# Performance work log

Hardware: AMD Instinct MI355X
Metric: run time of the kernel (lower is better)

The kernel has to match this reference:

```python
import jax, jax.numpy as jnp
import numpy as np

DN = ('NCHW', 'OIHW', 'NCHW')
EPS = 1e-5


def _conv(x, w, b, stride, pad):
    y = jax.lax.conv_general_dilated(x, w, (stride, stride), ((pad, pad), (pad, pad)), dimension_numbers=DN)
    return y + b[None, :, None, None]


def _convT(x, w, b):
    # PyTorch ConvTranspose2d(k=4, s=2, p=1); w: (Cin, Cout, 4, 4)
    k = jnp.flip(w, (2, 3)).transpose(1, 0, 2, 3)  # -> (Cout, Cin, 4, 4)
    y = jax.lax.conv_general_dilated(x, k, (1, 1), ((2, 2), (2, 2)), lhs_dilation=(2, 2), dimension_numbers=DN)
    return y + b[None, :, None, None]


def _bn(x, g, b):
    # training-mode BatchNorm2d: batch stats over (N, H, W)
    m = x.mean((0, 2, 3), keepdims=True)
    v = x.var((0, 2, 3), keepdims=True)
    return (x - m) * jax.lax.rsqrt(v + EPS) * g[None, :, None, None] + b[None, :, None, None]


def _resblock(x, g1, b1, w3, b3, g2, b2, w1, b1c):
    h = jax.nn.relu(_bn(x, g1, b1))
    h = _conv(h, w3, b3, 1, 1)
    h = jax.nn.relu(_bn(h, g2, b2))
    h = _conv(h, w1, b1c, 1, 0)
    return h + x


def setup_inputs() -> dict:
    B, C, H, W, D, K = 16, 3, 128, 128, 256, 512
    key = jax.random.key(0)
    ks = iter(jax.random.split(key, 16))
    s = 0.05
    inp = {
        'x': jax.random.normal(next(ks), (B, C, H, W), jnp.float32),
        'ec1_w': jax.random.normal(next(ks), (D, C, 4, 4), jnp.float32) * s,
        'ec1_b': jnp.zeros((D,), jnp.float32),
        'ebn1_g': jnp.ones((D,), jnp.float32),
        'ebn1_b': jnp.zeros((D,), jnp.float32),
        'ec2_w': jax.random.normal(next(ks), (D, D, 4, 4), jnp.float32) * s,
        'ec2_b': jnp.zeros((D,), jnp.float32),
        # 4 residual blocks stacked: [0,1]=encoder, [2,3]=decoder
        'rb_bn1_g': jnp.ones((4, D), jnp.float32),
        'rb_bn1_b': jnp.zeros((4, D), jnp.float32),
        'rb_c3_w': jax.random.normal(next(ks), (4, D, D, 3, 3), jnp.float32) * s,
        'rb_c3_b': jnp.zeros((4, D), jnp.float32),
        'rb_bn2_g': jnp.ones((4, D), jnp.float32),
        'rb_bn2_b': jnp.zeros((4, D), jnp.float32),
        'rb_c1_w': jax.random.normal(next(ks), (4, D, D, 1, 1), jnp.float32) * s,
        'rb_c1_b': jnp.zeros((4, D), jnp.float32),
        'dbn1_g': jnp.ones((D,), jnp.float32),
        'dbn1_b': jnp.zeros((D,), jnp.float32),
        'dct1_w': jax.random.normal(next(ks), (D, D, 4, 4), jnp.float32) * s,  # (Cin, Cout, kH, kW)
        'dct1_b': jnp.zeros((D,), jnp.float32),
        'dbn2_g': jnp.ones((D,), jnp.float32),
        'dbn2_b': jnp.zeros((D,), jnp.float32),
        'dct2_w': jax.random.normal(next(ks), (D, C, 4, 4), jnp.float32) * s,
        'dct2_b': jnp.zeros((C,), jnp.float32),
        'codebook': jax.random.uniform(next(ks), (K, D), jnp.float32, -1.0 / K, 1.0 / K),
    }
    return inp


def reference(x, ec1_w, ec1_b, ebn1_g, ebn1_b, ec2_w, ec2_b,
              rb_bn1_g, rb_bn1_b, rb_c3_w, rb_c3_b, rb_bn2_g, rb_bn2_b, rb_c1_w, rb_c1_b,
              dbn1_g, dbn1_b, dct1_w, dct1_b, dbn2_g, dbn2_b, dct2_w, dct2_b, codebook):
    def rb(h, i):
        return _resblock(h, rb_bn1_g[i], rb_bn1_b[i], rb_c3_w[i], rb_c3_b[i],
                         rb_bn2_g[i], rb_bn2_b[i], rb_c1_w[i], rb_c1_b[i])

    # Encoder
    h = _conv(x, ec1_w, ec1_b, 2, 1)
    h = jax.nn.relu(_bn(h, ebn1_g, ebn1_b))
    h = _conv(h, ec2_w, ec2_b, 2, 1)
    h = rb(h, 0)
    z_e = rb(h, 1)  # [N, D, H/4, W/4]

    # Vector quantizer: argmin_k sum_d (z - w_k)^2 via norm expansion
    N, D, Hh, Ww = z_e.shape
    ze_f = z_e.transpose(0, 2, 3, 1).reshape(-1, D)  # [M, D]
    d2 = ((ze_f ** 2).sum(1, keepdims=True)
          - 2.0 * ze_f @ codebook.T
          + (codebook ** 2).sum(1)[None, :])  # [M, K]
    q = jnp.argmin(d2, axis=1)
    z_q = codebook[q].reshape(N, Hh, Ww, D).transpose(0, 3, 1, 2)

    # Decoder (takes z_e, per original forward)
    d = rb(z_e, 2)
    d = rb(d, 3)
    d = jax.nn.relu(_bn(d, dbn1_g, dbn1_b))
    d = _convT(d, dct1_w, dct1_b)
    d = jax.nn.relu(_bn(d, dbn2_g, dbn2_b))
    x_rec = _convT(d, dct2_w, dct2_b)

    return (x_rec, z_e, z_q)
```

## Files before the change

### kernel.cpp

```cpp
#include <hip/hip_runtime.h>
#include <stdint.h>

typedef __bf16 bf16_t;
typedef __bf16 bf16x8 __attribute__((ext_vector_type(8)));
typedef float f32x4 __attribute__((ext_vector_type(4)));

#define DEVINL __device__ __forceinline__

DEVINL float bf2f(bf16_t h){ return (float)h; }
DEVINL bf16_t f2bf(float f){ return (bf16_t)f; }

DEVINL void g2l16(const void* g, void* l){
  __builtin_amdgcn_global_load_lds(
      (const __attribute__((address_space(1))) uint32_t*)g,
      (__attribute__((address_space(3))) uint32_t*)l, 16, 0, 0);
}

#define SB_BYTES    9469952
#define SB0_OFF     35684352
#define STATS_OFF   73564160
#define CBN_OFF     73586688
#define WP_OFF      73588736
#define XI_OFF      83353600
#define WS_NEEDED   91742208
#define WP_RB3(i) (1048576 + (i)*655360)
#define WP_RB1(i) (1048576 + (i)*655360 + 589824)
#define WP_CT     3670016
#define WP_CB     4718592
#define WP_EC1    4849664
#define WP_CT2    4866048
#define WP_ELEMS  4882432

DEVINL void zerohalo_one(bf16_t* buf, int IW, int idx){
  int g8 = idx & 31, r = idx >> 5;
  int H = 4*IW - 4;
  int nn = r / H, hp = r - nn*H;
  int y, x;
  if (hp < IW){ y = 0; x = hp; }
  else if (hp < 2*IW){ y = IW-1; x = hp - IW; }
  else {
    int h2 = hp - 2*IW;
    int side = h2 / (IW-2);
    int k = h2 - side*(IW-2);
    y = k + 1; x = side ? (IW-1) : 0;
  }
  bf16_t* p = buf + ((size_t)((nn*IW + y)*IW + x))*256 + g8*8;
  bf16x8 zv;
#pragma unroll
  for (int e = 0; e < 8; e++) zv[e] = f2bf(0.f);
  *(bf16x8*)p = zv;
}

__global__ __launch_bounds__(256) void k_prep(bf16_t* __restrict__ A64, bf16_t* __restrict__ SB,
                                              uint4* __restrict__ statz){
  int b = blockIdx.x, t = threadIdx.x;
  if (b < 521){
    int idx = b*256 + t;
    if (idx < 133120) zerohalo_one(A64, 66, idx);
  } else if (b < 1577){
    int r = b - 521;
    int buf = r / 264, li = r - buf*264;
    int idx = li*256 + t;
    if (idx < 67584) zerohalo_one(SB + (size_t)buf*(SB_BYTES/2), 34, idx);
  } else {
    int i = (b - 1577)*256 + t;
    if (i < 1408) statz[i] = make_uint4(0,0,0,0);
  }
}

__global__ __launch_bounds__(256) void k_repack(
    const float* __restrict__ ec2_w, const float* __restrict__ rb_c3_w,
    const float* __restrict__ rb_c1_w, const float* __restrict__ dct1_w,
    const float* __restrict__ codebook, const float* __restrict__ ec1_w,
    const float* __restrict__ dct2_w, bf16_t* __restrict__ wp, float* __restrict__ cbn)
{
  int idx = blockIdx.x*256 + threadIdx.x;
  if (idx >= WP_ELEMS){
    int k = idx - WP_ELEMS;
    if (k < 512){
      float s = 0.f;
      for (int d = 0; d < 256; d++){ float v = codebook[k*256 + d]; s += v*v; }
      cbn[k] = s;
    }
    return;
  }
  int l = idx; float v;
  if (l < 1048576) {
    int t = l>>16, co = (l>>8)&255, ci = l&255;
    v = ec2_w[co*4096 + ci*16 + t];
  } else {
    l -= 1048576;
    if (l < 2621440) {
      int i = l / 655360;
      int r = l - i*655360;
      if (r < 589824) {
        int t = r>>16, co = (r>>8)&255, ci = r&255;
        v = rb_c3_w[i*589824 + co*2304 + ci*9 + t];
      } else {
        r -= 589824;
        int co = r>>8, ci = r&255;
        v = rb_c1_w[i*65536 + co*256 + ci];
      }
    } else {
      l -= 2621440;
      if (l < 1048576) {
        int z = l>>18, r = l&262143, t = r>>16, co = (r>>8)&255, ci = r&255;
        int py = z>>1, px = z&1, a = t>>1, b = t&1;
        int ky = 2*a + 1 - py, kx = 2*b + 1 - px;
        v = dct1_w[ci*4096 + co*16 + ky*4 + kx];
      } else {
        l -= 1048576;
        if (l < 131072) {
          v = codebook[l];
        } else {
          l -= 131072;
          if (l < 16384){
            int co = l>>6, k = l&63;
            v = (k < 48) ? ec1_w[co*48 + k] : 0.f;
          } else {
            l -= 16384;
            int n = l>>8, ci = l&255;
            v = (n < 48) ? dct2_w[ci*48 + n] : 0.f;
          }
        }
      }
    }
  }
  wp[idx] = f2bf(v);
}

__global__ __launch_bounds__(256) void k_im2col(const float* __restrict__ x, bf16_t* __restrict__ Xi){
  int m = blockIdx.x*256 + threadIdx.x;
  int nn = m >> 12, oy = (m >> 6) & 63, ox = m & 63;
  bf16_t row[64];
#pragma unroll
  for (int k = 48; k < 64; k++) row[k] = f2bf(0.f);
#pragma unroll
  for (int ci = 0; ci < 3; ci++)
#pragma unroll
    for (int ky = 0; ky < 4; ky++){
      int iy = 2*oy + ky - 1;
      bool yok = (unsigned)iy < 128u;
#pragma unroll
      for (int kx = 0; kx < 4; kx++){
        int ix = 2*ox + kx - 1;
        float v = (yok && (unsigned)ix < 128u) ? x[((size_t)((nn*3+ci)*128 + iy))*128 + ix] : 0.f;
        row[ci*16 + ky*4 + kx] = f2bf(v);
      }
    }
#pragma unroll
  for (int u = 0; u < 8; u++){
    bf16x8 o;
#pragma unroll
    for (int e = 0; e < 8; e++) o[e] = row[u*8+e];
    *(bf16x8*)(Xi + (size_t)m*64 + u*8) = o;
  }
}

__global__ __launch_bounds__(256) void k_bnapply(const bf16_t* __restrict__ in, bf16_t* __restrict__ out,
    const float* __restrict__ stat, const float* __restrict__ g, const float* __restrict__ b,
    int hwlog, float invc)
{
  int idx = blockIdx.x*256 + threadIdx.x;
  int g8 = idx & 31, p = idx >> 5;
  int HW = 1 << hwlog, IW = HW + 2;
  int xx = p & (HW-1), yy = (p >> hwlog) & (HW-1), nn = p >> (2*hwlog);
  size_t a = ((size_t)((nn*IW + yy+1)*IW + xx+1))*256 + g8*8;
  float sm[8], sq[8], gv[8], bv[8];
#pragma unroll
  for (int e = 0; e < 8; e += 4){
    *(float4*)(sm+e) = *(const float4*)(stat + g8*8 + e);
    *(float4*)(sq+e) = *(const float4*)(stat + 256 + g8*8 + e);
    *(float4*)(gv+e) = *(const float4*)(g + g8*8 + e);
    *(float4*)(bv+e) = *(const float4*)(b + g8*8 + e);
  }
  bf16x8 v = *(const bf16x8*)(in + a);
  bf16x8 o;
#pragma unroll
  for (int e = 0; e < 8; e++){
    float mean = sm[e]*invc;
    float var  = sq[e]*invc - mean*mean;
    float sc = gv[e] * rsqrtf(var + 1e-5f);
    float sh = bv[e] - mean*sc;
    o[e] = f2bf(fmaxf(bf2f(v[e])*sc + sh, 0.f));
  }
  *(bf16x8*)(out + a) = o;
}

template<int MODE>
__global__ __launch_bounds__(256) void k_gemm(
    const bf16_t* __restrict__ in, const bf16_t* __restrict__ wp,
    const float* __restrict__ bias, const bf16_t* __restrict__ res,
    bf16_t* __restrict__ outb, float* __restrict__ outf,
    float* __restrict__ stat, int out_mode, float alpha)
{
  constexpr int TAPS = (MODE==0)?16:(MODE==1)?9:(MODE==3)?4:1;
  constexpr int CHUNKS = (MODE==5)?1:TAPS*4;
  const int N = gridDim.y * 64;

  __shared__ __align__(16) bf16_t As[128*64];
  __shared__ __align__(16) bf16_t Bs[64*64];
  __shared__ float s_sum[64], s_sum2[64];

  const int tid  = threadIdx.x;
  const int lane = tid & 63;
  const int wave = tid >> 6;
  const int m0   = blockIdx.x * 128;
  const int n0   = blockIdx.y * 64;
  int py = 0, px = 0;
  const bf16_t* wpp = wp;
  if (MODE == 3){ py = blockIdx.z >> 1; px = blockIdx.z & 1; wpp += (size_t)blockIdx.z * 262144; }

  int abase[4];
#pragma unroll
  for (int j = 0; j < 4; j++){
    int s = j*256 + wave*64 + lane;
    int row = s >> 3, ug = (s & 7) ^ (row & 7);
    int m = m0 + row;
    int pbase;
    if (MODE == 0){ int nn=m>>10, sp=m&1023, oy=sp>>5, ox=sp&31; pbase = (nn*66 + 2*oy)*66 + 2*ox; }
    else if (MODE == 3){ int nn=m>>10, sp=m&1023, oy=sp>>5, ox=sp&31; pbase = (nn*34 + oy+1+py)*34 + ox+1+px; }
    else if (MODE == 5){ pbase = 0; }
    else if (MODE == 6){ int nn=m>>12, oy=(m>>6)&63, ox=m&63; pbase = (nn*66 + oy+1)*66 + ox+1; }
    else { int nn=m>>10, sp=m&1023, oy=sp>>5, ox=sp&31; pbase = (nn*34 + oy)*34 + ox; }
    abase[j] = (MODE==5) ? (m*64 + ug*8) : (pbase*256 + ug*8);
  }
  int bbase[2];
#pragma unroll
  for (int j = 0; j < 2; j++){
    int s = j*256 + wave*64 + lane;
    int row = s >> 3, ug = (s & 7) ^ (row & 7);
    bbase[j] = (MODE==5) ? ((n0+row)*64 + ug*8) : ((n0+row)*256 + ug*8);
  }

  f32x4 acc[4][2];
#pragma unroll
  for (int i = 0; i < 4; i++)
#pragma unroll
    for (int j = 0; j < 2; j++) acc[i][j] = (f32x4){0.f,0.f,0.f,0.f};

  const int rowbase = (wave >> 1) * 64;
  const int colbase = (wave & 1) * 32;
  const int mf = lane & 15;
  const int kq = lane >> 4;

  for (int c = 0; c < CHUNKS; ++c){
    int t = (MODE==5) ? 0 : (c >> 2);
    int koff;
    if (MODE == 0)      koff = ((t >> 2)*66 + (t & 3))*256 + ((c&3)<<6);
    else if (MODE == 1){ int ky = t/3; koff = (ky*34 + (t - ky*3))*256 + ((c&3)<<6); }
    else if (MODE == 2) koff = 35*256 + ((c&3)<<6);
    else if (MODE == 3) koff = -((t >> 1)*34 + (t & 1))*256 + ((c&3)<<6);
    else if (MODE == 6) koff = ((c&3)<<6);
    else                koff = 0;
    size_t bko = (MODE==5) ? 0 : ((size_t)t*N*256 + ((c&3)<<6));
#pragma unroll
    for (int j = 0; j < 4; j++)
      g2l16(in + abase[j] + koff, As + (j*256 + wave*64)*8);
#pragma unroll
    for (int j = 0; j < 2; j++)
      g2l16(wpp + bko + bbase[j], Bs + (j*256 + wave*64)*8);
    __syncthreads();

#pragma unroll
    for (int kk = 0; kk < 2; kk++){
      bf16x8 af[4], bfr[2];
#pragma unroll
      for (int i = 0; i < 4; i++){
        int rr = rowbase + i*16 + mf;
        af[i] = *reinterpret_cast<const bf16x8*>(&As[rr*64 + (((kk*4+kq) ^ (rr&7))<<3)]);
      }
#pragma unroll
      for (int j = 0; j < 2; j++){
        int rr = colbase + j*16 + mf;
        bfr[j] = *reinterpret_cast<const bf16x8*>(&Bs[rr*64 + (((kk*4+kq) ^ (rr&7))<<3)]);
      }
#pragma unroll
      for (int i = 0; i < 4; i++)
#pragma unroll
        for (int j = 0; j < 2; j++)
          acc[i][j] = __builtin_amdgcn_mfma_f32_16x16x32_bf16(af[i], bfr[j], acc[i][j], 0, 0, 0);
    }
    __syncthreads();
  }

  float psum[2] = {0.f, 0.f}, psum2[2] = {0.f, 0.f};
  const int rowq = (lane >> 4) * 4;
#pragma unroll
  for (int i = 0; i < 4; i++){
#pragma unroll
    for (int r = 0; r < 4; r++){
      int m = m0 + rowbase + i*16 + rowq + r;
      int nn, oy, ox;
      if (MODE == 5){ nn = m >> 12; oy = (m >> 6) & 63; ox = m & 63; }
      else { nn = m >> 10; oy = (m >> 5) & 31; ox = m & 31; }
#pragma unroll
      for (int j = 0; j < 2; j++){
        int co = n0 + colbase + j*16 + mf;
        float v = alpha * acc[i][j][r] + (bias ? bias[co] : 0.f);
        if (res) v += bf2f(res[((size_t)((nn*34 + oy+1)*34 + ox+1))*256 + co]);
        psum[j] += v; psum2[j] += v*v;
        if (out_mode == 2){
          outf[(size_t)m * N + co] = v;
        } else if (MODE == 3){
          outb[((size_t)((nn*66 + 2*oy+py+1)*66 + 2*ox+px+1))*256 + co] = f2bf(v);
        } else if (MODE == 5){
          outb[((size_t)((nn*66 + oy+1)*66 + ox+1))*256 + co] = f2bf(v);
        } else {
          outb[((size_t)((nn*34 + oy+1)*34 + ox+1))*256 + co] = f2bf(v);
          if (out_mode == 1)
            outf[(size_t)nn*262144 + (size_t)co*1024 + oy*32 + ox] = v;
        }
      }
    }
  }
  if (stat){
    if (tid < 64){ s_sum[tid] = 0.f; s_sum2[tid] = 0.f; }
    __syncthreads();
#pragma unroll
    for (int j = 0; j < 2; j++){
      int cl = colbase + j*16 + mf;
      atomicAdd(&s_sum[cl], psum[j]);
      atomicAdd(&s_sum2[cl], psum2[j]);
    }
    __syncthreads();
    if (tid < 64){
      atomicAdd(&stat[n0 + tid], s_sum[tid]);
      atomicAdd(&stat[256 + n0 + tid], s_sum2[tid]);
    }
  }
}

__global__ __launch_bounds__(256) void k_vq_argmin(const float* __restrict__ scores,
    const float* __restrict__ cb, float* __restrict__ zq)
{
  __shared__ int best[32];
  __shared__ float Z[32*256];
  int tid = threadIdx.x, lane = tid & 63, wave = tid >> 6;
  int m0 = blockIdx.x * 32;
  int nn = m0 >> 10, y = (m0 >> 5) & 31;
  for (int rr = wave; rr < 32; rr += 4){
    const float* srow = scores + (size_t)(m0 + rr) * 512;
    float bv = 3.4e38f; int bk = 0;
    for (int k = lane; k < 512; k += 64){
      float v = srow[k];
      if (v < bv){ bv = v; bk = k; }
    }
    for (int off = 32; off; off >>= 1){
      float ov = __shfl_down(bv, off);
      int   ok = __shfl_down(bk, off);
      if (ov < bv || (ov == bv && ok < bk)){ bv = ov; bk = ok; }
    }
    if (lane == 0) best[rr] = bk;
  }
  __syncthreads();
  for (int rr = 0; rr < 32; rr++)
    Z[rr*256 + tid] = cb[best[rr]*256 + tid];
  __syncthreads();
  float* orow = zq + (size_t)nn*262144 + (size_t)tid*1024 + y*32;
#pragma unroll
  for (int x4 = 0; x4 < 8; x4++){
    float4 v;
    v.x = Z[(x4*4+0)*256 + tid];
    v.y = Z[(x4*4+1)*256 + tid];
    v.z = Z[(x4*4+2)*256 + tid];
    v.w = Z[(x4*4+3)*256 + tid];
    *(float4*)(orow + x4*4) = v;
  }
}

__global__ __launch_bounds__(256) void k_ct2asm(const float* __restrict__ P,
    const float* __restrict__ bias, float* __restrict__ out)
{
  int idx = blockIdx.x*256 + threadIdx.x;
  int nn = idx >> 14, oy2 = (idx >> 7) & 127, ox2 = idx & 127;
  int py = oy2 & 1, px = ox2 & 1, oyh = oy2 >> 1, oxh = ox2 >> 1;
  float a0 = bias[0], a1 = bias[1], a2 = bias[2];
#pragma unroll
  for (int a = 0; a < 2; a++){
    int iy = oyh + py - a;
    if ((unsigned)iy > 63u) continue;
    int ky = 2*a + 1 - py;
#pragma unroll
    for (int b = 0; b < 2; b++){
      int ix = oxh + px - b;
      if ((unsigned)ix > 63u) continue;
      int kx = 2*b + 1 - px;
      const float* pr = P + ((size_t)(nn*4096 + iy*64 + ix))*64 + ky*4 + kx;
      a0 += pr[0]; a1 += pr[16]; a2 += pr[32];
    }
  }
  size_t o = (size_t)nn*49152 + (size_t)oy2*128 + ox2;
  out[o]         = a0;
  out[o + 16384] = a1;
  out[o + 32768] = a2;
}

extern "C" void kernel_launch(void* const* d_in, const int* in_sizes, int n_in,
                              void* d_out, int out_size, void* d_ws, size_t ws_size,
                              hipStream_t stream)
{
  if (ws_size < (size_t)WS_NEEDED) return;

  const float* x       = (const float*)d_in[0];
  const float* ec1_w   = (const float*)d_in[1];
  const float* ec1_b   = (const float*)d_in[2];
  const float* ebn1_g  = (const float*)d_in[3];
  const float* ebn1_b  = (const float*)d_in[4];
  const float* ec2_w   = (const float*)d_in[5];
  const float* ec2_b   = (const float*)d_in[6];
  const float* rb_bn1_g= (const float*)d_in[7];
  const float* rb_bn1_b= (const float*)d_in[8];
  const float* rb_c3_w = (const float*)d_in[9];
  const float* rb_c3_b = (const float*)d_in[10];
  const float* rb_bn2_g= (const float*)d_in[11];
  const float* rb_bn2_b= (const float*)d_in[12];
  const float* rb_c1_w = (const float*)d_in[13];
  const float* rb_c1_b = (const float*)d_in[14];
  const float* dbn1_g  = (const float*)d_in[15];
  const float* dbn1_b  = (const float*)d_in[16];
  const float* dct1_w  = (const float*)d_in[17];
  const float* dct1_b  = (const float*)d_in[18];
  const float* dbn2_g  = (const float*)d_in[19];
  const float* dbn2_b  = (const float*)d_in[20];
  const float* dct2_w  = (const float*)d_in[21];
  const float* dct2_b  = (const float*)d_in[22];
  const float* codebook= (const float*)d_in[23];

  char* ws = (char*)d_ws;
  bf16_t* A64 = (bf16_t*)ws;
  float*  scores = (float*)ws;
  bf16_t* SB0 = (bf16_t*)(ws + SB0_OFF);
  bf16_t* SB1 = (bf16_t*)(ws + SB0_OFF + 1*SB_BYTES);
  bf16_t* SB2 = (bf16_t*)(ws + SB0_OFF + 2*SB_BYTES);
  bf16_t* SB3 = (bf16_t*)(ws + SB0_OFF + 3*SB_BYTES);
  float*  P   = (float*)(ws + SB0_OFF + 1*SB_BYTES);
  float*  stats = (float*)(ws + STATS_OFF);
  float*  cbn   = (float*)(ws + CBN_OFF);
  bf16_t* Wp    = (bf16_t*)(ws + WP_OFF);
  bf16_t* Xi    = (bf16_t*)(ws + XI_OFF);

  float* xrec = (float*)d_out;
  float* zef  = xrec + 786432;
  float* zqf  = zef + 4194304;

  k_prep  <<<dim3(1583),  256, 0, stream>>>(A64, SB0, (uint4*)(ws + STATS_OFF));
  k_repack<<<dim3(19074), 256, 0, stream>>>(ec2_w, rb_c3_w, rb_c1_w, dct1_w, codebook,
                                            ec1_w, dct2_w, Wp, cbn);

  k_im2col<<<dim3(256), 256, 0, stream>>>(x, Xi);
  k_gemm<5><<<dim3(512,4,1), 256, 0, stream>>>(Xi, Wp + WP_EC1, ec1_b, nullptr, A64, nullptr,
                                               stats, 0, 1.f);
  k_bnapply<<<dim3(8192), 256, 0, stream>>>(A64, A64, stats, ebn1_g, ebn1_b, 6, 1.f/65536.f);
  k_gemm<0><<<dim3(128,4,1), 256, 0, stream>>>(A64, Wp, ec2_b, nullptr, SB0, nullptr,
                                               stats + 1*512, 0, 1.f);

  auto launch_rb = [&](bf16_t* xin, bf16_t* xout, int i, int sIn, int sMid, int sOut, float* zf){
    k_bnapply<<<dim3(2048), 256, 0, stream>>>(xin, SB1, stats + sIn*512,
                                              rb_bn1_g + i*256, rb_bn1_b + i*256, 5, 1.f/16384.f);
    k_gemm<1><<<dim3(128,4,1), 256, 0, stream>>>(SB1, Wp + WP_RB3(i), rb_c3_b + i*256,
                                                 nullptr, SB2, nullptr, stats + sMid*512, 0, 1.f);
    k_bnapply<<<dim3(2048), 256, 0, stream>>>(SB2, SB2, stats + sMid*512,
                                              rb_bn2_g + i*256, rb_bn2_b + i*256, 5, 1.f/16384.f);
    k_gemm<2><<<dim3(128,4,1), 256, 0, stream>>>(SB2, Wp + WP_RB1(i), rb_c1_b + i*256,
                                                 xin, xout, zf, stats + sOut*512, zf ? 1 : 0, 1.f);
  };

  launch_rb(SB0, SB3, 0, 1, 2, 3, nullptr);
  launch_rb(SB3, SB0, 1, 3, 4, 5, zef);

  k_gemm<2><<<dim3(128,8,1), 256, 0, stream>>>(SB0, Wp + WP_CB, cbn, nullptr, nullptr, scores,
                                               nullptr, 2, -2.f);
  k_vq_argmin<<<dim3(512), 256, 0, stream>>>(scores, codebook, zqf);

  launch_rb(SB0, SB3, 2, 5, 6, 7, nullptr);
  launch_rb(SB3, SB0, 3, 7, 8, 9, nullptr);

  k_bnapply<<<dim3(2048), 256, 0, stream>>>(SB0, SB0, stats + 9*512, dbn1_g, dbn1_b, 5, 1.f/16384.f);
  k_gemm<3><<<dim3(128,4,4), 256, 0, stream>>>(SB0, Wp + WP_CT, dct1_b, nullptr, A64, nullptr,
                                               stats + 10*512, 0, 1.f);

  k_bnapply<<<dim3(8192), 256, 0, stream>>>(A64, A64, stats + 10*512, dbn2_g, dbn2_b, 6, 1.f/65536.f);
  k_gemm<6><<<dim3(512,1,1), 256, 0, stream>>>(A64, Wp + WP_CT2, nullptr, nullptr, nullptr, P,
                                               nullptr, 2, 1.f);
  k_ct2asm<<<dim3(1024), 256, 0, stream>>>(P, dct2_b, xrec);
}
```

Before: 733.8 us.

## Add halo-tiled implicit-GEMM conv kernel reusing LDS input across taps

Adds a k_conv kernel for the strided 4x4 conv, the 3x3 residual convs and the transposed conv. Each block stages a spatial input tile with its halo for one channel chunk in LDS once, then loops over all taps from that tile, instead of reloading the A tile from global memory for every tap. Weights are read straight from global memory into registers with a one-step prefetch rather than through LDS. k_gemm is reduced to the 1x1 and plain GEMM modes. The trade-offs are more LDS per block, a new XOR swizzle scheme and weight traffic that now hits global memory or cache on every tap.

```diff
diff --git a/kernel.cpp b/kernel.cpp
--- a/kernel.cpp
+++ b/kernel.cpp
@@ -188,14 +188,154 @@
 }
 
 template<int MODE>
+__global__ __launch_bounds__(256) void k_conv(
+    const bf16_t* __restrict__ in, const bf16_t* __restrict__ wp,
+    const float* __restrict__ bias, bf16_t* __restrict__ outb,
+    float* __restrict__ stat)
+{
+  constexpr int TAPS = (MODE==0)?16:(MODE==1)?9:4;
+  constexpr int UPP  = (MODE==0)?4:8;
+  constexpr int BK   = UPP*8;
+  constexpr int KK   = BK/32;
+  constexpr int NCH  = 256/BK;
+  constexpr int PXPAD= (MODE==0)?672:(MODE==1)?208:176;
+  constexpr int TU   = PXPAD*UPP;
+  constexpr int UPPL = (MODE==0)?2:3;
+
+  __shared__ __align__(16) bf16_t As[PXPAD*BK];
+  __shared__ float s_sum[64], s_sum2[64];
+
+  const int tid = threadIdx.x, lane = tid & 63, wave = tid >> 6;
+  const int nn = blockIdx.x >> 3, y0 = (blockIdx.x & 7) << 2;
+  const int n0 = blockIdx.y * 64;
+  int ppy = 0, ppx = 0;
+  const bf16_t* wpp = wp;
+  if (MODE == 3){ ppy = blockIdx.z >> 1; ppx = blockIdx.z & 1; wpp += (size_t)blockIdx.z * 262144; }
+
+  size_t wbase;
+  if (MODE == 0)      wbase = (size_t)((nn*66 + 2*y0)*66) * 256;
+  else if (MODE == 1) wbase = (size_t)((nn*34 + y0)*34) * 256;
+  else                wbase = (size_t)((nn*34 + y0 + ppy)*34) * 256;
+
+  const int rowbase = (wave >> 1) * 64;
+  const int colbase = (wave & 1) * 32;
+  const int mf = lane & 15;
+  const int kq = lane >> 4;
+
+  int pxb[4];
+#pragma unroll
+  for (int i = 0; i < 4; i++){
+    int ml = rowbase + i*16 + mf;
+    int yl = ml >> 5, xl = ml & 31;
+    if (MODE == 0)      pxb[i] = (2*yl)*66 + 2*xl;
+    else if (MODE == 1) pxb[i] = yl*34 + xl;
+    else                pxb[i] = (yl+1)*34 + xl + 1 + ppx;
+  }
+
+  f32x4 acc[4][2];
+#pragma unroll
+  for (int i = 0; i < 4; i++)
+#pragma unroll
+    for (int j = 0; j < 2; j++) acc[i][j] = (f32x4){0.f,0.f,0.f,0.f};
+
+  const bf16_t* bcol0 = wpp + (size_t)(n0 + colbase + mf)*256;
+
+  for (int c = 0; c < NCH; c++){
+    const int ch0 = c * BK;
+#pragma unroll
+    for (int g = 0; g < TU/64; g++){
+      int gg = g*64;
+      if ((gg & 255) != wave*64) continue;
+      int s = gg + lane;
+      int px = s >> UPPL, u = s & (UPP-1);
+      int key = (MODE == 0) ? ((px >> 1) & 3) : (px & 7);
+      g2l16(in + wbase + (size_t)px*256 + ch0 + ((u ^ key) << 3), As + (size_t)s*8);
+    }
+    bf16x8 b0c, b1c;
+    {
+      const bf16_t* bp = bcol0 + ch0 + (kq << 3);
+      b0c = *(const bf16x8*)bp;
+      b1c = *(const bf16x8*)(bp + 4096);
+    }
+    __syncthreads();
+#pragma unroll
+    for (int tk = 0; tk < TAPS*KK; tk++){
+      const int t = (KK == 2) ? (tk >> 1) : tk;
+      const int u = (KK == 2) ? ((tk & 1)*4 + kq) : kq;
+      bf16x8 b0n, b1n;
+      if (tk + 1 < TAPS*KK){
+        int t2 = (KK == 2) ? ((tk+1) >> 1) : (tk+1);
+        int u2 = (KK == 2) ? (((tk+1) & 1)*4 + kq) : kq;
+        const bf16_t* bp = bcol0 + (size_t)t2*65536 + ch0 + (u2 << 3);
+        b0n = *(const bf16x8*)bp;
+        b1n = *(const bf16x8*)(bp + 4096);
+      }
+      int to;
+      if (MODE == 0)      to = (t >> 2)*66 + (t & 3);
+      else if (MODE == 1) to = (t/3)*34 + (t - (t/3)*3);
+      else                to = -((t >> 1)*34 + (t & 1));
+      bf16x8 af[4];
+#pragma unroll
+      for (int i = 0; i < 4; i++){
+        int px = pxb[i] + to;
+        int key = (MODE == 0) ? ((px >> 1) & 3) : (px & 7);
+        af[i] = *reinterpret_cast<const bf16x8*>(&As[(size_t)px*BK + ((u ^ key) << 3)]);
+      }
+#pragma unroll
+      for (int i = 0; i < 4; i++){
+        acc[i][0] = __builtin_amdgcn_mfma_f32_16x16x32_bf16(af[i], b0c, acc[i][0], 0, 0, 0);
+        acc[i][1] = __builtin_amdgcn_mfma_f32_16x16x32_bf16(af[i], b1c, acc[i][1], 0, 0, 0);
+      }
+      b0c = b0n; b1c = b1n;
+    }
+    __syncthreads();
+  }
+
+  float psum[2] = {0.f, 0.f}, psum2[2] = {0.f, 0.f};
+  const int rowq = (lane >> 4) * 4;
+#pragma unroll
+  for (int i = 0; i < 4; i++){
+#pragma unroll
+    for (int r = 0; r < 4; r++){
+      int ml = rowbase + i*16 + rowq + r;
+      int y = y0 + (ml >> 5), x = ml & 31;
+#pragma unroll
+      for (int j = 0; j < 2; j++){
+        int co = n0 + colbase + j*16 + mf;
+        float v = acc[i][j][r] + bias[co];
+        psum[j] += v; psum2[j] += v*v;
+        if (MODE == 3)
+          outb[((size_t)((nn*66 + 2*y+ppy+1)*66 + 2*x+ppx+1))*256 + co] = f2bf(v);
+        else
+          outb[((size_t)((nn*34 + y+1)*34 + x+1))*256 + co] = f2bf(v);
+      }
+    }
+  }
+  if (stat){
+    if (tid < 64){ s_sum[tid] = 0.f; s_sum2[tid] = 0.f; }
+    __syncthreads();
+#pragma unroll
+    for (int j = 0; j < 2; j++){
+      int cl = colbase + j*16 + mf;
+      atomicAdd(&s_sum[cl], psum[j]);
+      atomicAdd(&s_sum2[cl], psum2[j]);
+    }
+    __syncthreads();
+    if (tid < 64){
+      atomicAdd(&stat[n0 + tid], s_sum[tid]);
+      atomicAdd(&stat[256 + n0 + tid], s_sum2[tid]);
+    }
+  }
+}
+
+template<int MODE>
 __global__ __launch_bounds__(256) void k_gemm(
     const bf16_t* __restrict__ in, const bf16_t* __restrict__ wp,
     const float* __restrict__ bias, const bf16_t* __restrict__ res,
     bf16_t* __restrict__ outb, float* __restrict__ outf,
     float* __restrict__ stat, int out_mode, float alpha)
 {
-  constexpr int TAPS = (MODE==0)?16:(MODE==1)?9:(MODE==3)?4:1;
-  constexpr int CHUNKS = (MODE==5)?1:TAPS*4;
+  constexpr int CHUNKS = (MODE==5)?1:4;
   const int N = gridDim.y * 64;
 
   __shared__ __align__(16) bf16_t As[128*64];
@@ -207,9 +347,6 @@
   const int wave = tid >> 6;
   const int m0   = blockIdx.x * 128;
   const int n0   = blockIdx.y * 64;
-  int py = 0, px = 0;
-  const bf16_t* wpp = wp;
-  if (MODE == 3){ py = blockIdx.z >> 1; px = blockIdx.z & 1; wpp += (size_t)blockIdx.z * 262144; }
 
   int abase[4];
 #pragma unroll
@@ -218,11 +355,9 @@
     int row = s >> 3, ug = (s & 7) ^ (row & 7);
     int m = m0 + row;
     int pbase;
-    if (MODE == 0){ int nn=m>>10, sp=m&1023, oy=sp>>5, ox=sp&31; pbase = (nn*66 + 2*oy)*66 + 2*ox; }
-    else if (MODE == 3){ int nn=m>>10, sp=m&1023, oy=sp>>5, ox=sp&31; pbase = (nn*34 + oy+1+py)*34 + ox+1+px; }
-    else if (MODE == 5){ pbase = 0; }
+    if (MODE == 5){ pbase = 0; }
     else if (MODE == 6){ int nn=m>>12, oy=(m>>6)&63, ox=m&63; pbase = (nn*66 + oy+1)*66 + ox+1; }
-    else { int nn=m>>10, sp=m&1023, oy=sp>>5, ox=sp&31; pbase = (nn*34 + oy)*34 + ox; }
+    else { int nn=m>>10, sp=m&1023, oy=sp>>5, ox=sp&31; pbase = (nn*34 + oy+1)*34 + ox+1; }
     abase[j] = (MODE==5) ? (m*64 + ug*8) : (pbase*256 + ug*8);
   }
   int bbase[2];
@@ -245,21 +380,13 @@
   const int kq = lane >> 4;
 
   for (int c = 0; c < CHUNKS; ++c){
-    int t = (MODE==5) ? 0 : (c >> 2);
-    int koff;
-    if (MODE == 0)      koff = ((t >> 2)*66 + (t & 3))*256 + ((c&3)<<6);
-    else if (MODE == 1){ int ky = t/3; koff = (ky*34 + (t - ky*3))*256 + ((c&3)<<6); }
-    else if (MODE == 2) koff = 35*256 + ((c&3)<<6);
-    else if (MODE == 3) koff = -((t >> 1)*34 + (t & 1))*256 + ((c&3)<<6);
-    else if (MODE == 6) koff = ((c&3)<<6);
-    else                koff = 0;
-    size_t bko = (MODE==5) ? 0 : ((size_t)t*N*256 + ((c&3)<<6));
+    int koff = (MODE==5) ? 0 : (c<<6);
 #pragma unroll
     for (int j = 0; j < 4; j++)
       g2l16(in + abase[j] + koff, As + (j*256 + wave*64)*8);
 #pragma unroll
     for (int j = 0; j < 2; j++)
-      g2l16(wpp + bko + bbase[j], Bs + (j*256 + wave*64)*8);
+      g2l16(wp + koff + bbase[j], Bs + (j*256 + wave*64)*8);
     __syncthreads();
 
 #pragma unroll
@@ -302,8 +429,6 @@
         psum[j] += v; psum2[j] += v*v;
         if (out_mode == 2){
           outf[(size_t)m * N + co] = v;
-        } else if (MODE == 3){
-          outb[((size_t)((nn*66 + 2*oy+py+1)*66 + 2*ox+px+1))*256 + co] = f2bf(v);
         } else if (MODE == 5){
           outb[((size_t)((nn*66 + oy+1)*66 + ox+1))*256 + co] = f2bf(v);
         } else {
@@ -452,14 +577,13 @@
   k_gemm<5><<<dim3(512,4,1), 256, 0, stream>>>(Xi, Wp + WP_EC1, ec1_b, nullptr, A64, nullptr,
                                                stats, 0, 1.f);
   k_bnapply<<<dim3(8192), 256, 0, stream>>>(A64, A64, stats, ebn1_g, ebn1_b, 6, 1.f/65536.f);
-  k_gemm<0><<<dim3(128,4,1), 256, 0, stream>>>(A64, Wp, ec2_b, nullptr, SB0, nullptr,
-                                               stats + 1*512, 0, 1.f);
+  k_conv<0><<<dim3(128,4), 256, 0, stream>>>(A64, Wp, ec2_b, SB0, stats + 1*512);
 
   auto launch_rb = [&](bf16_t* xin, bf16_t* xout, int i, int sIn, int sMid, int sOut, float* zf){
     k_bnapply<<<dim3(2048), 256, 0, stream>>>(xin, SB1, stats + sIn*512,
                                               rb_bn1_g + i*256, rb_bn1_b + i*256, 5, 1.f/16384.f);
-    k_gemm<1><<<dim3(128,4,1), 256, 0, stream>>>(SB1, Wp + WP_RB3(i), rb_c3_b + i*256,
-                                                 nullptr, SB2, nullptr, stats + sMid*512, 0, 1.f);
+    k_conv<1><<<dim3(128,4), 256, 0, stream>>>(SB1, Wp + WP_RB3(i), rb_c3_b + i*256,
+                                               SB2, stats + sMid*512);
     k_bnapply<<<dim3(2048), 256, 0, stream>>>(SB2, SB2, stats + sMid*512,
                                               rb_bn2_g + i*256, rb_bn2_b + i*256, 5, 1.f/16384.f);
     k_gemm<2><<<dim3(128,4,1), 256, 0, stream>>>(SB2, Wp + WP_RB1(i), rb_c1_b + i*256,
@@ -477,8 +601,7 @@
   launch_rb(SB3, SB0, 3, 7, 8, 9, nullptr);
 
   k_bnapply<<<dim3(2048), 256, 0, stream>>>(SB0, SB0, stats + 9*512, dbn1_g, dbn1_b, 5, 1.f/16384.f);
-  k_gemm<3><<<dim3(128,4,4), 256, 0, stream>>>(SB0, Wp + WP_CT, dct1_b, nullptr, A64, nullptr,
-                                               stats + 10*512, 0, 1.f);
+  k_conv<3><<<dim3(128,4,4), 256, 0, stream>>>(SB0, Wp + WP_CT, dct1_b, A64, stats + 10*512);
 
   k_bnapply<<<dim3(8192), 256, 0, stream>>>(A64, A64, stats + 10*512, dbn2_g, dbn2_b, 6, 1.f/65536.f);
   k_gemm<6><<<dim3(512,1,1), 256, 0, stream>>>(A64, Wp + WP_CT2, nullptr, nullptr, nullptr, P,
```

After: 779.3 us. 6.2% more time.

## Double-buffer GEMM LDS tiles to overlap global loads with MFMA

Applied to the files above, without the earlier changes.

Splits the A and B shared-memory tiles into two buffers. The next chunk's global-to-LDS loads are issued before computing on the current chunk, and completion is tracked with explicit vmcnt waits and raw barriers instead of __syncthreads. Tap offset computation moves into a staging lambda, and the MODE 2 centre offset is folded into abase. The aim is to hide global load latency behind the matrix instructions, at the cost of doubled LDS per block and possibly lower occupancy. It also changes MODE 6 epilogue indexing to a 64x64 spatial layout.

```diff
diff --git a/kernel.cpp b/kernel.cpp
--- a/kernel.cpp
+++ b/kernel.cpp
@@ -198,8 +198,8 @@
   constexpr int CHUNKS = (MODE==5)?1:TAPS*4;
   const int N = gridDim.y * 64;
 
-  __shared__ __align__(16) bf16_t As[128*64];
-  __shared__ __align__(16) bf16_t Bs[64*64];
+  __shared__ __align__(16) bf16_t As[2][128*64];
+  __shared__ __align__(16) bf16_t Bs[2][64*64];
   __shared__ float s_sum[64], s_sum2[64];
 
   const int tid  = threadIdx.x;
@@ -207,9 +207,9 @@
   const int wave = tid >> 6;
   const int m0   = blockIdx.x * 128;
   const int n0   = blockIdx.y * 64;
-  int py = 0, px = 0;
+  int ppy = 0, ppx = 0;
   const bf16_t* wpp = wp;
-  if (MODE == 3){ py = blockIdx.z >> 1; px = blockIdx.z & 1; wpp += (size_t)blockIdx.z * 262144; }
+  if (MODE == 3){ ppy = blockIdx.z >> 1; ppx = blockIdx.z & 1; wpp += (size_t)blockIdx.z * 262144; }
 
   int abase[4];
 #pragma unroll
@@ -219,10 +219,11 @@
     int m = m0 + row;
     int pbase;
     if (MODE == 0){ int nn=m>>10, sp=m&1023, oy=sp>>5, ox=sp&31; pbase = (nn*66 + 2*oy)*66 + 2*ox; }
-    else if (MODE == 3){ int nn=m>>10, sp=m&1023, oy=sp>>5, ox=sp&31; pbase = (nn*34 + oy+1+py)*34 + ox+1+px; }
+    else if (MODE == 1){ int nn=m>>10, sp=m&1023, oy=sp>>5, ox=sp&31; pbase = (nn*34 + oy)*34 + ox; }
+    else if (MODE == 3){ int nn=m>>10, sp=m&1023, oy=sp>>5, ox=sp&31; pbase = (nn*34 + oy+1+ppy)*34 + ox+1+ppx; }
     else if (MODE == 5){ pbase = 0; }
     else if (MODE == 6){ int nn=m>>12, oy=(m>>6)&63, ox=m&63; pbase = (nn*66 + oy+1)*66 + ox+1; }
-    else { int nn=m>>10, sp=m&1023, oy=sp>>5, ox=sp&31; pbase = (nn*34 + oy)*34 + ox; }
+    else { int nn=m>>10, sp=m&1023, oy=sp>>5, ox=sp&31; pbase = (nn*34 + oy+1)*34 + ox+1; }
     abase[j] = (MODE==5) ? (m*64 + ug*8) : (pbase*256 + ug*8);
   }
   int bbase[2];
@@ -233,6 +234,22 @@
     bbase[j] = (MODE==5) ? ((n0+row)*64 + ug*8) : ((n0+row)*256 + ug*8);
   }
 
+  auto stage = [&](int buf, int c){
+    int t = c >> 2;
+    int koff, bko;
+    if (MODE == 0){ koff = ((t>>2)*66 + (t&3))*256 + ((c&3)<<6); bko = t*65536 + ((c&3)<<6); }
+    else if (MODE == 1){ int ky = t/3; koff = (ky*34 + (t - ky*3))*256 + ((c&3)<<6); bko = t*65536 + ((c&3)<<6); }
+    else if (MODE == 3){ koff = -(((t>>1)*34 + (t&1))*256) + ((c&3)<<6); bko = t*65536 + ((c&3)<<6); }
+    else if (MODE == 5){ koff = 0; bko = 0; }
+    else { koff = (c&3)<<6; bko = (c&3)<<6; }
+#pragma unroll
+    for (int j = 0; j < 4; j++)
+      g2l16(in + abase[j] + koff, &As[buf][(j*256 + wave*64)*8]);
+#pragma unroll
+    for (int j = 0; j < 2; j++)
+      g2l16(wpp + bko + bbase[j], &Bs[buf][(j*256 + wave*64)*8]);
+  };
+
   f32x4 acc[4][2];
 #pragma unroll
   for (int i = 0; i < 4; i++)
@@ -244,23 +261,16 @@
   const int mf = lane & 15;
   const int kq = lane >> 4;
 
+  stage(0, 0);
   for (int c = 0; c < CHUNKS; ++c){
-    int t = (MODE==5) ? 0 : (c >> 2);
-    int koff;
-    if (MODE == 0)      koff = ((t >> 2)*66 + (t & 3))*256 + ((c&3)<<6);
-    else if (MODE == 1){ int ky = t/3; koff = (ky*34 + (t - ky*3))*256 + ((c&3)<<6); }
-    else if (MODE == 2) koff = 35*256 + ((c&3)<<6);
-    else if (MODE == 3) koff = -((t >> 1)*34 + (t & 1))*256 + ((c&3)<<6);
-    else if (MODE == 6) koff = ((c&3)<<6);
-    else                koff = 0;
-    size_t bko = (MODE==5) ? 0 : ((size_t)t*N*256 + ((c&3)<<6));
-#pragma unroll
-    for (int j = 0; j < 4; j++)
-      g2l16(in + abase[j] + koff, As + (j*256 + wave*64)*8);
-#pragma unroll
-    for (int j = 0; j < 2; j++)
-      g2l16(wpp + bko + bbase[j], Bs + (j*256 + wave*64)*8);
-    __syncthreads();
+    const int cur = c & 1;
+    if (c + 1 < CHUNKS){
+      stage(cur ^ 1, c + 1);
+      asm volatile("s_waitcnt vmcnt(6)" ::: "memory");
+    } else {
+      asm volatile("s_waitcnt vmcnt(0)" ::: "memory");
+    }
+    asm volatile("s_barrier" ::: "memory");
 
 #pragma unroll
     for (int kk = 0; kk < 2; kk++){
@@ -268,12 +278,12 @@
 #pragma unroll
       for (int i = 0; i < 4; i++){
         int rr = rowbase + i*16 + mf;
-        af[i] = *reinterpret_cast<const bf16x8*>(&As[rr*64 + (((kk*4+kq) ^ (rr&7))<<3)]);
+        af[i] = *reinterpret_cast<const bf16x8*>(&As[cur][rr*64 + (((kk*4+kq) ^ (rr&7))<<3)]);
       }
 #pragma unroll
       for (int j = 0; j < 2; j++){
         int rr = colbase + j*16 + mf;
-        bfr[j] = *reinterpret_cast<const bf16x8*>(&Bs[rr*64 + (((kk*4+kq) ^ (rr&7))<<3)]);
+        bfr[j] = *reinterpret_cast<const bf16x8*>(&Bs[cur][rr*64 + (((kk*4+kq) ^ (rr&7))<<3)]);
       }
 #pragma unroll
       for (int i = 0; i < 4; i++)
@@ -281,7 +291,7 @@
         for (int j = 0; j < 2; j++)
           acc[i][j] = __builtin_amdgcn_mfma_f32_16x16x32_bf16(af[i], bfr[j], acc[i][j], 0, 0, 0);
     }
-    __syncthreads();
+    asm volatile("s_barrier" ::: "memory");
   }
 
   float psum[2] = {0.f, 0.f}, psum2[2] = {0.f, 0.f};
@@ -292,7 +302,7 @@
     for (int r = 0; r < 4; r++){
       int m = m0 + rowbase + i*16 + rowq + r;
       int nn, oy, ox;
-      if (MODE == 5){ nn = m >> 12; oy = (m >> 6) & 63; ox = m & 63; }
+      if (MODE == 5 || MODE == 6){ nn = m >> 12; oy = (m >> 6) & 63; ox = m & 63; }
       else { nn = m >> 10; oy = (m >> 5) & 31; ox = m & 31; }
 #pragma unroll
       for (int j = 0; j < 2; j++){
@@ -303,7 +313,7 @@
         if (out_mode == 2){
           outf[(size_t)m * N + co] = v;
         } else if (MODE == 3){
-          outb[((size_t)((nn*66 + 2*oy+py+1)*66 + 2*ox+px+1))*256 + co] = f2bf(v);
+          outb[((size_t)((nn*66 + 2*oy+ppy+1)*66 + 2*ox+ppx+1))*256 + co] = f2bf(v);
         } else if (MODE == 5){
           outb[((size_t)((nn*66 + oy+1)*66 + ox+1))*256 + co] = f2bf(v);
         } else {
```

Measured after the change: 738.0 us. No clear change (+0.6%).
